# Kernel optimization log

Hardware: AMD Instinct MI355X
Metric: run time of the kernel (lower is better)

## Reference

```python
import jax, jax.numpy as jnp
import numpy as np

T = 8  # number of DP iterations (self.T)

def setup_inputs() -> dict:
    key = jax.random.key(0)
    ks = jax.random.split(key, 9)
    bs, dims, L, d = 16, 4, 2048, 256
    x = jax.random.uniform(ks[0], (bs, dims, L), dtype=jnp.float32)  # one-hot-like input
    s_in = 1.0 / np.sqrt(dims)
    s_d = 1.0 / np.sqrt(d)
    W1 = jax.random.uniform(ks[1], (d, dims), minval=-s_in, maxval=s_in, dtype=jnp.float32)
    b1 = jax.random.uniform(ks[2], (d,), minval=-s_in, maxval=s_in, dtype=jnp.float32)
    W2 = jax.random.uniform(ks[3], (d, d), minval=-s_d, maxval=s_d, dtype=jnp.float32)
    b2 = jax.random.uniform(ks[4], (d,), minval=-s_d, maxval=s_d, dtype=jnp.float32)
    W3 = jax.random.uniform(ks[5], (d, dims), minval=-s_in, maxval=s_in, dtype=jnp.float32)
    b3 = jax.random.uniform(ks[6], (d,), minval=-s_in, maxval=s_in, dtype=jnp.float32)
    W4 = jax.random.uniform(ks[7], (d, d), minval=-s_d, maxval=s_d, dtype=jnp.float32)
    b4 = jax.random.uniform(ks[8], (d,), minval=-s_d, maxval=s_d, dtype=jnp.float32)
    return dict(x=x, W1=W1, b1=b1, W2=W2, b2=b2, W3=W3, b3=b3, W4=W4, b4=b4)

def reference(x, W1, b1, W2, b2, W3, b3, W4, b4):
    # x: (bs, dims, L). The original allocates V:(bs,T+1,L+2,L+2,d) but only the
    # two diagonals V[i,j,j+1] ("up") and V[i,j,j-1] ("down") are ever written/read,
    # so the recurrence collapses to two (bs,L,d) lanes.
    a = jnp.einsum('bdl,od->blo', x, W1) + b1  # W1(x_j) for all j: (bs, L, d)
    bs, L, d = a.shape
    zcol = jnp.zeros((bs, 1, d), a.dtype)
    shift_r = lambda v: jnp.concatenate([zcol, v[:, :-1]], axis=1)  # v[j-1], zero at j=0
    shift_l = lambda v: jnp.concatenate([v[:, 1:], zcol], axis=1)   # v[j+1], zero at j=L-1
    up = jnp.zeros_like(a)   # up[j]   = V[i, j+1, j+2] (0-indexed lane)
    down = jnp.zeros_like(a) # down[j] = V[i, j+1, j]
    for _ in range(T):
        up = jax.nn.relu(a + shift_r(up) @ W2.T + b2)
        down = jax.nn.relu(a + shift_l(down) @ W2.T + b2)
    c = jnp.einsum('bdl,od->blo', x, W3) + b3
    # miu[j] = relu(W3 x_j + W4(V[T,j-1,j]) + W4(V[T,j+1,j]))
    miu = jax.nn.relu(c + (shift_r(up) @ W4.T + b4) + (shift_l(down) @ W4.T + b4))
    return miu  # (bs, L, d)
```

## Files before the change

kernel.cpp:

```cpp
#include <hip/hip_runtime.h>


typedef __bf16 bf16x8 __attribute__((ext_vector_type(8)));
typedef __bf16 bf16x4 __attribute__((ext_vector_type(4)));
typedef float f32x16 __attribute__((ext_vector_type(16)));
typedef unsigned int uint2v __attribute__((ext_vector_type(2)));

#define MFMA32(a, b, c) __builtin_amdgcn_mfma_f32_32x32x16_bf16(a, b, c, 0, 0, 0)

__device__ __forceinline__ unsigned short f2bf(float f) {
  unsigned int u = __builtin_bit_cast(unsigned int, f);
  u += 0x7fffu + ((u >> 16) & 1u);
  return (unsigned short)(u >> 16);
}

__device__ __forceinline__ unsigned pk2(float a, float b) {
  return (unsigned)f2bf(a) | ((unsigned)f2bf(b) << 16);
}

__global__ void prep_kernel(const float* __restrict__ W1, const float* __restrict__ b1,
                            const float* __restrict__ W2, const float* __restrict__ b2,
                            const float* __restrict__ W3, const float* __restrict__ b3,
                            const float* __restrict__ W4, const float* __restrict__ b4,
                            unsigned short* __restrict__ ws) {
  int t8 = blockIdx.x * 256 + threadIdx.x;
  if (t8 >= 17408) return;
  int idx = t8 * 8;
  int4 outv;
  if (idx < 131072) {
    const float* W = (idx < 65536) ? W2 : W4;
    int f = (idx & 65535) >> 3;
    int lane = f & 63, slot = f >> 6;
    int ks = slot & 15, ot = slot >> 4;
    int o = ot * 32 + (lane & 31);
    int kbase = ks * 16 + (lane >> 5) * 8;
    const float4* row = (const float4*)(W + o * 256 + kbase);
    float4 v0 = row[0];
    float4 v1 = row[1];
    outv = make_int4((int)pk2(v0.x, v0.y), (int)pk2(v0.z, v0.w),
                     (int)pk2(v1.x, v1.y), (int)pk2(v1.z, v1.w));
  } else {
    int i = idx - 131072;
    bool first = (i < 4096);
    int f = (i & 4095) >> 3;
    int lane = f & 63, ot = f >> 6;
    int o = ot * 32 + (lane & 31);
    outv = make_int4(0, 0, 0, 0);
    if (lane < 32) {
      const float4 wrow = *(const float4*)((first ? W1 : W3) + o * 4);
      float bias = first ? (b1[o] + b2[o]) : (b3[o] + 2.0f * b4[o]);
      outv = make_int4((int)pk2(wrow.x, wrow.y), (int)pk2(wrow.z, wrow.w),
                       (int)pk2(bias, 0.0f), 0);
    }
  }
  *(int4*)(ws + idx) = outv;
}

#define NC 10

#define LOAD_AF(AF, S0) { \
    int ka_ = (4 * w + NC + (S0)) & 15; \
    AF[0][0] = __builtin_bit_cast(bf16x8, w2f[(ot0 * 16 + ka_) * 64 + l]); \
    AF[0][1] = __builtin_bit_cast(bf16x8, w2f[((ot0 + 1) * 16 + ka_) * 64 + l]); \
    int kb_ = (4 * w + NC + (S0) + 1) & 15; \
    AF[1][0] = __builtin_bit_cast(bf16x8, w2f[(ot0 * 16 + kb_) * 64 + l]); \
    AF[1][1] = __builtin_bit_cast(bf16x8, w2f[((ot0 + 1) * 16 + kb_) * 64 + l]); }

#define GSTEP(RB, KSR, A0, A1) { \
    bf16x8 bu_ = __builtin_bit_cast(bf16x8, (RB)[(2 * (KSR) + khalf) * 32 + lane31]); \
    acc[0] = MFMA32(A0, bu_, acc[0]); \
    acc[1] = MFMA32(A1, bu_, acc[1]); }

#define SELFSTEP(ZK, S) { \
    bf16x8 bu_ = __builtin_bit_cast(bf16x8, ZK[(S) >> 1][(S) & 1]); \
    acc[0] = MFMA32(w2c[0][S], bu_, acc[0]); \
    acc[1] = MFMA32(w2c[1][S], bu_, acc[1]); }

#define PACKZ(ZK) { \
    _Pragma("unroll") for (int t2 = 0; t2 < 2; ++t2) { \
      unsigned lo[4], hi[4]; \
      _Pragma("unroll") for (int q = 0; q < 4; ++q) { \
        bf16x4 h; \
        h.x = (__bf16)fmaxf(acc[t2][4 * q + 0], 0.0f); \
        h.y = (__bf16)fmaxf(acc[t2][4 * q + 1], 0.0f); \
        h.z = (__bf16)fmaxf(acc[t2][4 * q + 2], 0.0f); \
        h.w = (__bf16)fmaxf(acc[t2][4 * q + 3], 0.0f); \
        uint2 u = __builtin_bit_cast(uint2, h); \
        lo[q] = u.x; hi[q] = u.y; \
      } \
      uint2v r0 = __builtin_amdgcn_permlane32_swap(lo[0], lo[1], false, false); \
      uint2v r1 = __builtin_amdgcn_permlane32_swap(hi[0], hi[1], false, false); \
      ZK[t2][0] = make_int4((int)r0.x, (int)r1.x, (int)r0.y, (int)r1.y); \
      uint2v r2 = __builtin_amdgcn_permlane32_swap(lo[2], lo[3], false, false); \
      uint2v r3 = __builtin_amdgcn_permlane32_swap(hi[2], hi[3], false, false); \
      ZK[t2][1] = make_int4((int)r2.x, (int)r3.x, (int)r2.y, (int)r3.y); \
    } }

#define WRITEZ(ZK, WB) { \
    _Pragma("unroll") for (int t2 = 0; t2 < 2; ++t2) \
    _Pragma("unroll") for (int p = 0; p < 2; ++p) \
      (WB)[((ot0 + t2) * 4 + 2 * p + khalf) * 32 + lane31] = ZK[t2][p]; }

#define XWSTEP(PH, T) { \
    int widx_ = (PH) == 0 ? (lane31 + (T) - 1) : (lane31 + 17 - (T)); \
    const int4* p_ = (l < 32) ? (xw + widx_) : (&zc); \
    bf16x8 bx_ = __builtin_bit_cast(bf16x8, *p_); \
    acc[0] = MFMA32(w1x[0], bx_, acc[0]); \
    acc[1] = MFMA32(w1x[1], bx_, acc[1]); }

#define INTERVAL_G(PH, T, RB, WB, ZK) { \
  bf16x8 afA[2][2], afB[2][2], afC[2][2]; \
  LOAD_AF(afA, 0) \
  f32x16 acc[2] = {}; \
  XWSTEP(PH, T) \
  __builtin_amdgcn_s_setprio(1); \
  SELFSTEP(ZK, 0) SELFSTEP(ZK, 1) SELFSTEP(ZK, 2) SELFSTEP(ZK, 3) \
  LOAD_AF(afB, 2) \
  GSTEP(RB, (4 * w + 4) & 15, w2c[0][4], w2c[1][4]) \
  GSTEP(RB, (4 * w + 5) & 15, w2c[0][5], w2c[1][5]) \
  GSTEP(RB, (4 * w + 6) & 15, w2c[0][6], w2c[1][6]) \
  GSTEP(RB, (4 * w + 7) & 15, w2c[0][7], w2c[1][7]) \
  GSTEP(RB, (4 * w + 8) & 15, w2c[0][8], w2c[1][8]) \
  GSTEP(RB, (4 * w + 9) & 15, w2c[0][9], w2c[1][9]) \
  GSTEP(RB, (4 * w + 10) & 15, afA[0][0], afA[0][1]) \
  GSTEP(RB, (4 * w + 11) & 15, afA[1][0], afA[1][1]) \
  LOAD_AF(afC, 4) \
  GSTEP(RB, (4 * w + 12) & 15, afB[0][0], afB[0][1]) \
  GSTEP(RB, (4 * w + 13) & 15, afB[1][0], afB[1][1]) \
  GSTEP(RB, (4 * w + 14) & 15, afC[0][0], afC[0][1]) \
  GSTEP(RB, (4 * w + 15) & 15, afC[1][0], afC[1][1]) \
  __builtin_amdgcn_s_setprio(0); \
  PACKZ(ZK) \
  WRITEZ(ZK, WB) }

#define INTERVAL_P(PH, WB, ZK) { \
  f32x16 acc[2] = {}; \
  XWSTEP(PH, 1) \
  PACKZ(ZK) \
  WRITEZ(ZK, WB) }

__global__ __launch_bounds__(256, 2)
void chain_kernel(const float* __restrict__ x, const unsigned short* __restrict__ ws,
                  float* __restrict__ out) {
  __shared__ int4 UA[2][1024];
  __shared__ int4 UB[2][1024];
  __shared__ int4 xw[48];
  __shared__ int4 zc;

  const int tid = threadIdx.x;
  const int l = tid & 63;
  const int w = tid >> 6;
  const int lane31 = l & 31;
  const int khalf = l >> 5;
  const int tile = blockIdx.x;
  const int b = tile >> 6;
  const int j0 = (tile & 63) * 32;

  const int4* w2f = (const int4*)ws;
  const int4* w4f = (const int4*)(ws + 65536);
  const int4* w1xg = (const int4*)(ws + 131072);
  const int4* w3xg = (const int4*)(ws + 135168);

  if (tid == 0) zc = make_int4(0, 0, 0, 0);
  if (tid < 48) {
    int j = j0 - 8 + tid;
    int4 c = make_int4(0, 0, 0, 0);
    if (j >= 0 && j < 2048) {
      const float* xb = x + (b * 4) * 2048 + j;
      unsigned short h0 = f2bf(xb[0]);
      unsigned short h1 = f2bf(xb[2048]);
      unsigned short h2 = f2bf(xb[4096]);
      unsigned short h3 = f2bf(xb[6144]);
      c = make_int4((int)(h0 | ((unsigned int)h1 << 16)),
                    (int)(h2 | ((unsigned int)h3 << 16)),
                    0x00003f80, 0);
    }
    xw[tid] = c;
  }

  const int ot0 = w * 2;
  bf16x8 w2c[2][NC];
  bf16x8 w1x[2];
#pragma unroll
  for (int t2 = 0; t2 < 2; ++t2) {
    w1x[t2] = __builtin_bit_cast(bf16x8, w1xg[(ot0 + t2) * 64 + l]);
#pragma unroll
    for (int i = 0; i < NC; ++i) {
      int ksr = (4 * w + i) & 15;
      w2c[t2][i] = __builtin_bit_cast(bf16x8, w2f[((ot0 + t2) * 16 + ksr) * 64 + l]);
    }
  }
  __syncthreads();

  int4 zkU[2][2], zkD[2][2];

  INTERVAL_P(0, UA[0], zkU)
  INTERVAL_P(1, UB[0], zkD)
  __syncthreads();

#pragma unroll 1
  for (int k = 1; k < 8; ++k) {
    const int4* ra = UA[(k - 1) & 1];
    int4* wa = UA[k & 1];
    const int4* rb = UB[(k - 1) & 1];
    int4* wb = UB[k & 1];
    const int T = k + 1;
    INTERVAL_G(0, T, ra, wa, zkU)
    INTERVAL_G(1, T, rb, wb, zkD)
    __syncthreads();
  }

  {
    f32x16 acc[2] = {};
    { int widx = lane31 + 8;
      const int4* p_ = (l < 32) ? (xw + widx) : (&zc);
      bf16x8 bx = __builtin_bit_cast(bf16x8, *p_);
      bf16x8 w3x0 = __builtin_bit_cast(bf16x8, w3xg[ot0 * 64 + l]);
      bf16x8 w3x1 = __builtin_bit_cast(bf16x8, w3xg[(ot0 + 1) * 64 + l]);
      acc[0] = MFMA32(w3x0, bx, acc[0]);
      acc[1] = MFMA32(w3x1, bx, acc[1]); }
    __builtin_amdgcn_s_setprio(1);
#pragma unroll 1
    for (int ph = 0; ph < 2; ++ph) {
      const int4* Sp = ph ? UB[1] : UA[1];
      const int4* zz = ph ? &zkD[0][0] : &zkU[0][0];
#pragma unroll
      for (int s = 0; s < 4; ++s) {
        int ksr = 4 * w + s;
        bf16x8 af0 = __builtin_bit_cast(bf16x8, w4f[(ot0 * 16 + ksr) * 64 + l]);
        bf16x8 af1 = __builtin_bit_cast(bf16x8, w4f[((ot0 + 1) * 16 + ksr) * 64 + l]);
        bf16x8 bu = __builtin_bit_cast(bf16x8, zz[s]);
        acc[0] = MFMA32(af0, bu, acc[0]);
        acc[1] = MFMA32(af1, bu, acc[1]);
      }
#pragma unroll
      for (int i = 4; i < 16; ++i) {
        int ksr = (4 * w + i) & 15;
        bf16x8 af0 = __builtin_bit_cast(bf16x8, w4f[(ot0 * 16 + ksr) * 64 + l]);
        bf16x8 af1 = __builtin_bit_cast(bf16x8, w4f[((ot0 + 1) * 16 + ksr) * 64 + l]);
        bf16x8 bu = __builtin_bit_cast(bf16x8, Sp[(2 * ksr + khalf) * 32 + lane31]);
        acc[0] = MFMA32(af0, bu, acc[0]);
        acc[1] = MFMA32(af1, bu, acc[1]);
      }
    }
    __builtin_amdgcn_s_setprio(0);
    int pbase = (b * 2048 + j0 + lane31) * 256;
#pragma unroll
    for (int t2 = 0; t2 < 2; ++t2) {
#pragma unroll
      for (int q = 0; q < 4; ++q) {
        int ob = (ot0 + t2) * 32 + 8 * q + 4 * khalf;
        float4 v;
        v.x = fmaxf(acc[t2][4 * q + 0], 0.0f);
        v.y = fmaxf(acc[t2][4 * q + 1], 0.0f);
        v.z = fmaxf(acc[t2][4 * q + 2], 0.0f);
        v.w = fmaxf(acc[t2][4 * q + 3], 0.0f);
        *(float4*)(out + pbase + ob) = v;
      }
    }
  }
}

extern "C" void kernel_launch(void* const* d_in, const int* in_sizes, int n_in,
                              void* d_out, int out_size, void* d_ws, size_t ws_size,
                              hipStream_t stream) {
  const float* x  = (const float*)d_in[0];
  const float* W1 = (const float*)d_in[1];
  const float* b1 = (const float*)d_in[2];
  const float* W2 = (const float*)d_in[3];
  const float* b2 = (const float*)d_in[4];
  const float* W3 = (const float*)d_in[5];
  const float* b3 = (const float*)d_in[6];
  const float* W4 = (const float*)d_in[7];
  const float* b4 = (const float*)d_in[8];
  unsigned short* ws = (unsigned short*)d_ws;

  prep_kernel<<<68, 256, 0, stream>>>(W1, b1, W2, b2, W3, b3, W4, b4, ws);
  chain_kernel<<<1024, 256, 0, stream>>>(x, ws, (float*)d_out);
}
```

Measured before the change: 128.5 us.

## Split output tiles across 8 waves, one 32-row tile per wave

Each block now runs 512 threads (8 waves) instead of 256, and each wave owns one 32-wide output tile instead of two. This halves the MFMAs and register-resident W2 fragments per wave. The register cache of W2 shrinks from 10 to 4 k-slices, with the remaining A fragments streamed from global/L2 in a rotating triple buffer. The aim is more wave-level parallelism on the serial 8-step chain and a shorter critical path per interval, at the cost of more global weight loads per step and larger block barriers.

```diff
diff --git a/kernel.cpp b/kernel.cpp
--- a/kernel.cpp
+++ b/kernel.cpp
@@ -56,90 +56,86 @@
   *(int4*)(ws + idx) = outv;
 }
 
-#define NC 10
-
-#define LOAD_AF(AF, S0) { \
-    int ka_ = (4 * w + NC + (S0)) & 15; \
-    AF[0][0] = __builtin_bit_cast(bf16x8, w2f[(ot0 * 16 + ka_) * 64 + l]); \
-    AF[0][1] = __builtin_bit_cast(bf16x8, w2f[((ot0 + 1) * 16 + ka_) * 64 + l]); \
-    int kb_ = (4 * w + NC + (S0) + 1) & 15; \
-    AF[1][0] = __builtin_bit_cast(bf16x8, w2f[(ot0 * 16 + kb_) * 64 + l]); \
-    AF[1][1] = __builtin_bit_cast(bf16x8, w2f[((ot0 + 1) * 16 + kb_) * 64 + l]); }
-
-#define GSTEP(RB, KSR, A0, A1) { \
+
+#define LOAD_AF(AF, I) { \
+    int ka_ = (2 * w + (I)) & 15; \
+    AF[0] = __builtin_bit_cast(bf16x8, w2f[(ot * 16 + ka_) * 64 + l]); \
+    int kb_ = (2 * w + (I) + 1) & 15; \
+    AF[1] = __builtin_bit_cast(bf16x8, w2f[(ot * 16 + kb_) * 64 + l]); }
+
+#define GSTEP(RB, KSR, A0) { \
     bf16x8 bu_ = __builtin_bit_cast(bf16x8, (RB)[(2 * (KSR) + khalf) * 32 + lane31]); \
-    acc[0] = MFMA32(A0, bu_, acc[0]); \
-    acc[1] = MFMA32(A1, bu_, acc[1]); }
+    acc = MFMA32(A0, bu_, acc); }
 
 #define SELFSTEP(ZK, S) { \
-    bf16x8 bu_ = __builtin_bit_cast(bf16x8, ZK[(S) >> 1][(S) & 1]); \
-    acc[0] = MFMA32(w2c[0][S], bu_, acc[0]); \
-    acc[1] = MFMA32(w2c[1][S], bu_, acc[1]); }
+    bf16x8 bu_ = __builtin_bit_cast(bf16x8, ZK[S]); \
+    acc = MFMA32(w2c[S], bu_, acc); }
 
 #define PACKZ(ZK) { \
-    _Pragma("unroll") for (int t2 = 0; t2 < 2; ++t2) { \
-      unsigned lo[4], hi[4]; \
-      _Pragma("unroll") for (int q = 0; q < 4; ++q) { \
-        bf16x4 h; \
-        h.x = (__bf16)fmaxf(acc[t2][4 * q + 0], 0.0f); \
-        h.y = (__bf16)fmaxf(acc[t2][4 * q + 1], 0.0f); \
-        h.z = (__bf16)fmaxf(acc[t2][4 * q + 2], 0.0f); \
-        h.w = (__bf16)fmaxf(acc[t2][4 * q + 3], 0.0f); \
-        uint2 u = __builtin_bit_cast(uint2, h); \
-        lo[q] = u.x; hi[q] = u.y; \
-      } \
-      uint2v r0 = __builtin_amdgcn_permlane32_swap(lo[0], lo[1], false, false); \
-      uint2v r1 = __builtin_amdgcn_permlane32_swap(hi[0], hi[1], false, false); \
-      ZK[t2][0] = make_int4((int)r0.x, (int)r1.x, (int)r0.y, (int)r1.y); \
-      uint2v r2 = __builtin_amdgcn_permlane32_swap(lo[2], lo[3], false, false); \
-      uint2v r3 = __builtin_amdgcn_permlane32_swap(hi[2], hi[3], false, false); \
-      ZK[t2][1] = make_int4((int)r2.x, (int)r3.x, (int)r2.y, (int)r3.y); \
-    } }
+    unsigned lo[4], hi[4]; \
+    _Pragma("unroll") for (int q = 0; q < 4; ++q) { \
+      bf16x4 h; \
+      h.x = (__bf16)fmaxf(acc[4 * q + 0], 0.0f); \
+      h.y = (__bf16)fmaxf(acc[4 * q + 1], 0.0f); \
+      h.z = (__bf16)fmaxf(acc[4 * q + 2], 0.0f); \
+      h.w = (__bf16)fmaxf(acc[4 * q + 3], 0.0f); \
+      uint2 u = __builtin_bit_cast(uint2, h); \
+      lo[q] = u.x; hi[q] = u.y; \
+    } \
+    uint2v r0 = __builtin_amdgcn_permlane32_swap(lo[0], lo[1], false, false); \
+    uint2v r1 = __builtin_amdgcn_permlane32_swap(hi[0], hi[1], false, false); \
+    ZK[0] = make_int4((int)r0.x, (int)r1.x, (int)r0.y, (int)r1.y); \
+    uint2v r2 = __builtin_amdgcn_permlane32_swap(lo[2], lo[3], false, false); \
+    uint2v r3 = __builtin_amdgcn_permlane32_swap(hi[2], hi[3], false, false); \
+    ZK[1] = make_int4((int)r2.x, (int)r3.x, (int)r2.y, (int)r3.y); }
 
 #define WRITEZ(ZK, WB) { \
-    _Pragma("unroll") for (int t2 = 0; t2 < 2; ++t2) \
-    _Pragma("unroll") for (int p = 0; p < 2; ++p) \
-      (WB)[((ot0 + t2) * 4 + 2 * p + khalf) * 32 + lane31] = ZK[t2][p]; }
+    (WB)[(ot * 4 + khalf) * 32 + lane31] = ZK[0]; \
+    (WB)[(ot * 4 + 2 + khalf) * 32 + lane31] = ZK[1]; }
 
 #define XWSTEP(PH, T) { \
     int widx_ = (PH) == 0 ? (lane31 + (T) - 1) : (lane31 + 17 - (T)); \
     const int4* p_ = (l < 32) ? (xw + widx_) : (&zc); \
     bf16x8 bx_ = __builtin_bit_cast(bf16x8, *p_); \
-    acc[0] = MFMA32(w1x[0], bx_, acc[0]); \
-    acc[1] = MFMA32(w1x[1], bx_, acc[1]); }
+    acc = MFMA32(w1x, bx_, acc); }
 
 #define INTERVAL_G(PH, T, RB, WB, ZK) { \
-  bf16x8 afA[2][2], afB[2][2], afC[2][2]; \
-  LOAD_AF(afA, 0) \
-  f32x16 acc[2] = {}; \
+  bf16x8 afA[2], afB[2], afC[2]; \
+  LOAD_AF(afA, 4) \
+  f32x16 acc = {}; \
   XWSTEP(PH, T) \
   __builtin_amdgcn_s_setprio(1); \
-  SELFSTEP(ZK, 0) SELFSTEP(ZK, 1) SELFSTEP(ZK, 2) SELFSTEP(ZK, 3) \
-  LOAD_AF(afB, 2) \
-  GSTEP(RB, (4 * w + 4) & 15, w2c[0][4], w2c[1][4]) \
-  GSTEP(RB, (4 * w + 5) & 15, w2c[0][5], w2c[1][5]) \
-  GSTEP(RB, (4 * w + 6) & 15, w2c[0][6], w2c[1][6]) \
-  GSTEP(RB, (4 * w + 7) & 15, w2c[0][7], w2c[1][7]) \
-  GSTEP(RB, (4 * w + 8) & 15, w2c[0][8], w2c[1][8]) \
-  GSTEP(RB, (4 * w + 9) & 15, w2c[0][9], w2c[1][9]) \
-  GSTEP(RB, (4 * w + 10) & 15, afA[0][0], afA[0][1]) \
-  GSTEP(RB, (4 * w + 11) & 15, afA[1][0], afA[1][1]) \
-  LOAD_AF(afC, 4) \
-  GSTEP(RB, (4 * w + 12) & 15, afB[0][0], afB[0][1]) \
-  GSTEP(RB, (4 * w + 13) & 15, afB[1][0], afB[1][1]) \
-  GSTEP(RB, (4 * w + 14) & 15, afC[0][0], afC[0][1]) \
-  GSTEP(RB, (4 * w + 15) & 15, afC[1][0], afC[1][1]) \
+  SELFSTEP(ZK, 0) SELFSTEP(ZK, 1) \
+  LOAD_AF(afB, 6) \
+  GSTEP(RB, (2 * w + 2) & 15, w2c[2]) \
+  GSTEP(RB, (2 * w + 3) & 15, w2c[3]) \
+  LOAD_AF(afC, 8) \
+  GSTEP(RB, (2 * w + 4) & 15, afA[0]) \
+  GSTEP(RB, (2 * w + 5) & 15, afA[1]) \
+  LOAD_AF(afA, 10) \
+  GSTEP(RB, (2 * w + 6) & 15, afB[0]) \
+  GSTEP(RB, (2 * w + 7) & 15, afB[1]) \
+  LOAD_AF(afB, 12) \
+  GSTEP(RB, (2 * w + 8) & 15, afC[0]) \
+  GSTEP(RB, (2 * w + 9) & 15, afC[1]) \
+  LOAD_AF(afC, 14) \
+  GSTEP(RB, (2 * w + 10) & 15, afA[0]) \
+  GSTEP(RB, (2 * w + 11) & 15, afA[1]) \
+  GSTEP(RB, (2 * w + 12) & 15, afB[0]) \
+  GSTEP(RB, (2 * w + 13) & 15, afB[1]) \
+  GSTEP(RB, (2 * w + 14) & 15, afC[0]) \
+  GSTEP(RB, (2 * w + 15) & 15, afC[1]) \
   __builtin_amdgcn_s_setprio(0); \
   PACKZ(ZK) \
   WRITEZ(ZK, WB) }
 
 #define INTERVAL_P(PH, WB, ZK) { \
-  f32x16 acc[2] = {}; \
+  f32x16 acc = {}; \
   XWSTEP(PH, 1) \
   PACKZ(ZK) \
   WRITEZ(ZK, WB) }
 
-__global__ __launch_bounds__(256, 2)
+__global__ __launch_bounds__(512, 4)
 void chain_kernel(const float* __restrict__ x, const unsigned short* __restrict__ ws,
                   float* __restrict__ out) {
   __shared__ int4 UA[2][1024];
@@ -150,6 +146,7 @@
   const int tid = threadIdx.x;
   const int l = tid & 63;
   const int w = tid >> 6;
+  const int ot = w;
   const int lane31 = l & 31;
   const int khalf = l >> 5;
   const int tile = blockIdx.x;
@@ -178,21 +175,17 @@
     xw[tid] = c;
   }
 
-  const int ot0 = w * 2;
-  bf16x8 w2c[2][NC];
-  bf16x8 w1x[2];
-#pragma unroll
-  for (int t2 = 0; t2 < 2; ++t2) {
-    w1x[t2] = __builtin_bit_cast(bf16x8, w1xg[(ot0 + t2) * 64 + l]);
-#pragma unroll
-    for (int i = 0; i < NC; ++i) {
-      int ksr = (4 * w + i) & 15;
-      w2c[t2][i] = __builtin_bit_cast(bf16x8, w2f[((ot0 + t2) * 16 + ksr) * 64 + l]);
-    }
+  bf16x8 w2c[4];
+  bf16x8 w1x;
+  w1x = __builtin_bit_cast(bf16x8, w1xg[ot * 64 + l]);
+#pragma unroll
+  for (int i = 0; i < 4; ++i) {
+    int ksr = (2 * w + i) & 15;
+    w2c[i] = __builtin_bit_cast(bf16x8, w2f[(ot * 16 + ksr) * 64 + l]);
   }
   __syncthreads();
 
-  int4 zkU[2][2], zkD[2][2];
+  int4 zkU[2], zkD[2];
 
   INTERVAL_P(0, UA[0], zkU)
   INTERVAL_P(1, UB[0], zkD)
@@ -211,52 +204,43 @@
   }
 
   {
-    f32x16 acc[2] = {};
+    f32x16 acc = {};
     { int widx = lane31 + 8;
       const int4* p_ = (l < 32) ? (xw + widx) : (&zc);
       bf16x8 bx = __builtin_bit_cast(bf16x8, *p_);
-      bf16x8 w3x0 = __builtin_bit_cast(bf16x8, w3xg[ot0 * 64 + l]);
-      bf16x8 w3x1 = __builtin_bit_cast(bf16x8, w3xg[(ot0 + 1) * 64 + l]);
-      acc[0] = MFMA32(w3x0, bx, acc[0]);
-      acc[1] = MFMA32(w3x1, bx, acc[1]); }
+      bf16x8 w3x = __builtin_bit_cast(bf16x8, w3xg[ot * 64 + l]);
+      acc = MFMA32(w3x, bx, acc); }
     __builtin_amdgcn_s_setprio(1);
 #pragma unroll 1
     for (int ph = 0; ph < 2; ++ph) {
       const int4* Sp = ph ? UB[1] : UA[1];
-      const int4* zz = ph ? &zkD[0][0] : &zkU[0][0];
-#pragma unroll
-      for (int s = 0; s < 4; ++s) {
-        int ksr = 4 * w + s;
-        bf16x8 af0 = __builtin_bit_cast(bf16x8, w4f[(ot0 * 16 + ksr) * 64 + l]);
-        bf16x8 af1 = __builtin_bit_cast(bf16x8, w4f[((ot0 + 1) * 16 + ksr) * 64 + l]);
+      const int4* zz = ph ? zkD : zkU;
+#pragma unroll
+      for (int s = 0; s < 2; ++s) {
+        int ksr = 2 * w + s;
+        bf16x8 af = __builtin_bit_cast(bf16x8, w4f[(ot * 16 + ksr) * 64 + l]);
         bf16x8 bu = __builtin_bit_cast(bf16x8, zz[s]);
-        acc[0] = MFMA32(af0, bu, acc[0]);
-        acc[1] = MFMA32(af1, bu, acc[1]);
+        acc = MFMA32(af, bu, acc);
       }
 #pragma unroll
-      for (int i = 4; i < 16; ++i) {
-        int ksr = (4 * w + i) & 15;
-        bf16x8 af0 = __builtin_bit_cast(bf16x8, w4f[(ot0 * 16 + ksr) * 64 + l]);
-        bf16x8 af1 = __builtin_bit_cast(bf16x8, w4f[((ot0 + 1) * 16 + ksr) * 64 + l]);
+      for (int i = 2; i < 16; ++i) {
+        int ksr = (2 * w + i) & 15;
+        bf16x8 af = __builtin_bit_cast(bf16x8, w4f[(ot * 16 + ksr) * 64 + l]);
         bf16x8 bu = __builtin_bit_cast(bf16x8, Sp[(2 * ksr + khalf) * 32 + lane31]);
-        acc[0] = MFMA32(af0, bu, acc[0]);
-        acc[1] = MFMA32(af1, bu, acc[1]);
+        acc = MFMA32(af, bu, acc);
       }
     }
     __builtin_amdgcn_s_setprio(0);
     int pbase = (b * 2048 + j0 + lane31) * 256;
 #pragma unroll
-    for (int t2 = 0; t2 < 2; ++t2) {
-#pragma unroll
-      for (int q = 0; q < 4; ++q) {
-        int ob = (ot0 + t2) * 32 + 8 * q + 4 * khalf;
-        float4 v;
-        v.x = fmaxf(acc[t2][4 * q + 0], 0.0f);
-        v.y = fmaxf(acc[t2][4 * q + 1], 0.0f);
-        v.z = fmaxf(acc[t2][4 * q + 2], 0.0f);
-        v.w = fmaxf(acc[t2][4 * q + 3], 0.0f);
-        *(float4*)(out + pbase + ob) = v;
-      }
+    for (int q = 0; q < 4; ++q) {
+      int ob = ot * 32 + 8 * q + 4 * khalf;
+      float4 v;
+      v.x = fmaxf(acc[4 * q + 0], 0.0f);
+      v.y = fmaxf(acc[4 * q + 1], 0.0f);
+      v.z = fmaxf(acc[4 * q + 2], 0.0f);
+      v.w = fmaxf(acc[4 * q + 3], 0.0f);
+      *(float4*)(out + pbase + ob) = v;
     }
   }
 }
@@ -276,5 +260,5 @@
   unsigned short* ws = (unsigned short*)d_ws;
 
   prep_kernel<<<68, 256, 0, stream>>>(W1, b1, W2, b2, W3, b3, W4, b4, ws);
-  chain_kernel<<<1024, 256, 0, stream>>>(x, ws, (float*)d_out);
-}
+  chain_kernel<<<1024, 512, 0, stream>>>(x, ws, (float*)d_out);
+}
```

Measured after the change: 131.0 us. Within noise of the previous version (+1.9%).
